# Kernel optimization log

Measured on AMD Instinct MI355X. Metric: run time of the kernel, lower is better.

Reference implementation:

```python
import jax, jax.numpy as jnp
import numpy as np

Vx, Vy, B, N, C, H, M_VIEWS = 8, 8, 4, 196, 768, 12, 4
DH = C // H
SCALE = DH ** -0.5
HID = 4 * C


def _layer_norm(x, w, b, eps=1e-5):
    mu = jnp.mean(x, axis=-1, keepdims=True)
    var = jnp.mean((x - mu) ** 2, axis=-1, keepdims=True)
    return (x - mu) / jnp.sqrt(var + eps) * w + b


def setup_inputs() -> dict:
    key = jax.random.key(0)
    ks = jax.random.split(key, 32)
    s = 0.02
    inp = {
        "xs": jax.random.normal(ks[0], (Vx, B, N, C), jnp.float32),
        "ys": jax.random.normal(ks[1], (Vy, B, N, C), jnp.float32),
        "xposes": jax.random.randint(ks[2], (Vx, B, N, 2), 0, N),
        "yposes": jax.random.randint(ks[3], (Vy, B, N, 2), 0, N),
        "rel_ids": jax.random.randint(ks[4], (Vx * M_VIEWS,), 0, Vy),
        "M": M_VIEWS,
        # self-attention params (qkv_bias=False, proj has bias)
        "qkv_w": jax.random.normal(ks[5], (3 * C, C), jnp.float32) * s,
        "attn_proj_w": jax.random.normal(ks[6], (C, C), jnp.float32) * s,
        "attn_proj_b": jnp.zeros((C,), jnp.float32),
        # cross-attention params
        "q_w": jax.random.normal(ks[7], (C, C), jnp.float32) * s,
        "k_w": jax.random.normal(ks[8], (C, C), jnp.float32) * s,
        "v_w": jax.random.normal(ks[9], (C, C), jnp.float32) * s,
        "cross_proj_w": jax.random.normal(ks[10], (C, C), jnp.float32) * s,
        "cross_proj_b": jnp.zeros((C,), jnp.float32),
        # MLP
        "fc1_w": jax.random.normal(ks[11], (HID, C), jnp.float32) * s,
        "fc1_b": jnp.zeros((HID,), jnp.float32),
        "fc2_w": jax.random.normal(ks[12], (C, HID), jnp.float32) * s,
        "fc2_b": jnp.zeros((C,), jnp.float32),
        # layer norms
        "ln1_w": jnp.ones((C,), jnp.float32), "ln1_b": jnp.zeros((C,), jnp.float32),
        "ln2_w": jnp.ones((C,), jnp.float32), "ln2_b": jnp.zeros((C,), jnp.float32),
        "ln3_w": jnp.ones((C,), jnp.float32), "ln3_b": jnp.zeros((C,), jnp.float32),
        "lny_w": jnp.ones((C,), jnp.float32), "lny_b": jnp.zeros((C,), jnp.float32),
    }
    return inp


def _forward(xs, ys, rel_ids, M,
             qkv_w, attn_proj_w, attn_proj_b,
             q_w, k_w, v_w, cross_proj_w, cross_proj_b,
             fc1_w, fc1_b, fc2_w, fc2_b,
             ln1_w, ln1_b, ln2_w, ln2_b, ln3_w, ln3_b, lny_w, lny_b):
    vx, b, nx, c = xs.shape
    vy, _, ny, _ = ys.shape
    x = xs.reshape(vx * b, nx, c)

    # ---- self-attention over each target view (rope=None) ----
    h = _layer_norm(x, ln1_w, ln1_b)
    qkv = (h @ qkv_w.T).reshape(vx * b, nx, 3, H, DH)
    q = jnp.transpose(qkv[:, :, 0], (0, 2, 1, 3))  # (VB,H,N,dh)
    k = jnp.transpose(qkv[:, :, 1], (0, 2, 1, 3))
    v = jnp.transpose(qkv[:, :, 2], (0, 2, 1, 3))
    attn = jax.nn.softmax(jnp.einsum('bhnd,bhkd->bhnk', q, k) * SCALE, axis=-1)
    o = jnp.einsum('bhnk,bhkd->bnhd', attn, v).reshape(vx * b, nx, c)
    x = x + (o @ attn_proj_w.T + attn_proj_b)

    # ---- batched multi-view cross-attention ----
    xn = _layer_norm(x.reshape(vx, b, nx, c), ln2_w, ln2_b)
    yn = _layer_norm(ys, lny_w, lny_b)
    qs = (xn @ q_w.T).reshape(vx, b, nx, H, DH)
    ks = (yn @ k_w.T).reshape(vy, b, ny, H, DH)
    vs = (yn @ v_w.T).reshape(vy, b, ny, H, DH)
    ks_r = ks[rel_ids].reshape(vx, M, b, ny, H, DH)  # index_select + group
    vs_r = vs[rel_ids].reshape(vx, M, b, ny, H, DH)
    # q is broadcast across the M group dim (no materialized expand)
    scores = jnp.einsum('vbnhd,vmbkhd->vmbhnk', qs, ks_r) * SCALE
    a = jax.nn.softmax(scores, axis=-1)
    o = jnp.einsum('vmbhnk,vmbkhd->vmbnhd', a, vs_r).reshape(vx, M, b, nx, c)
    o = o @ cross_proj_w.T + cross_proj_b  # (Vx,M,B,Nx,C)
    merged = jnp.max(o, axis=1).reshape(vx * b, nx, c)  # max-merge over M
    x = x + merged

    # ---- MLP ----
    h = _layer_norm(x, ln3_w, ln3_b)
    x = x + (jax.nn.gelu(h @ fc1_w.T + fc1_b, approximate=False) @ fc2_w.T + fc2_b)
    return x.reshape(vx, b, nx, c)


def reference(xs, ys, xposes, yposes, rel_ids, M,
              qkv_w, attn_proj_w, attn_proj_b,
              q_w, k_w, v_w, cross_proj_w, cross_proj_b,
              fc1_w, fc1_b, fc2_w, fc2_b,
              ln1_w, ln1_b, ln2_w, ln2_b, ln3_w, ln3_b, lny_w, lny_b):
    # xposes/yposes unused because rope=None in this configuration
    return _forward(xs, ys, rel_ids, M,
                    qkv_w, attn_proj_w, attn_proj_b,
                    q_w, k_w, v_w, cross_proj_w, cross_proj_b,
                    fc1_w, fc1_b, fc2_w, fc2_b,
                    ln1_w, ln1_b, ln2_w, ln2_b, ln3_w, ln3_b, lny_w, lny_b)
```

## Files before the change

### kernel.cpp

```cpp
#include <hip/hip_runtime.h>
#include <hip/hip_bf16.h>
#include <stdint.h>
#include <math.h>

#define H_ 12
#define NQ 196
#define CD 768
#define HIDD 3072
#define VX 8
#define VY 8
#define BB 4
#define MV 4
#define VBB 32
#define ROWS 6272
#define CROSS_ROWS 25088
#define SCALE_LOG2E 0.180336880260608f

typedef __attribute__((ext_vector_type(8))) short short8;
typedef __attribute__((ext_vector_type(4))) float f32x4;
typedef __attribute__((ext_vector_type(4))) unsigned short u16x4;
typedef unsigned short u16;

#define AS1 __attribute__((address_space(1)))
#define AS3 __attribute__((address_space(3)))

__device__ __forceinline__ float bf2f(u16 u){
  union { unsigned int i; float f; } v; v.i = ((unsigned int)u) << 16; return v.f;
}
__device__ __forceinline__ u16 f2bf(float f){
  union { unsigned int i; float f; } v; v.f = f;
  return (u16)((v.i + 0x7fff + ((v.i >> 16) & 1)) >> 16);
}
__device__ __forceinline__ unsigned int f2u(float f){
  union { unsigned int i; float f; } v; v.f = f; return v.i;
}

struct CastSegs {
  const float* src[7];
  u16* dst[7];
  int cum[8];
};
__global__ __launch_bounds__(256) void k_cast_all(CastSegs segs){
  int i = blockIdx.x * 256 + threadIdx.x;
  if (i >= segs.cum[7]) return;
  int s = 0;
  #pragma unroll
  for (int k = 1; k < 7; k++) s += (i >= segs.cum[k]);
  const int off = i - segs.cum[s];
  segs.dst[s][off] = f2bf(segs.src[s][off]);
}

__global__ __launch_bounds__(256) void k_ln_bf16(const float* __restrict__ x,
    const float* __restrict__ w, const float* __restrict__ b,
    u16* __restrict__ out){
  const int row = blockIdx.x;
  const int tid = threadIdx.x;
  const float* xr = x + (size_t)row * CD;
  float v0 = xr[tid], v1 = xr[tid + 256], v2 = xr[tid + 512];
  float s  = v0 + v1 + v2;
  float s2 = v0*v0 + v1*v1 + v2*v2;
  __shared__ float red[8];
  const int lane = tid & 63, wid = tid >> 6;
  #pragma unroll
  for (int o = 32; o; o >>= 1){ s += __shfl_down(s, o); s2 += __shfl_down(s2, o); }
  if (lane == 0){ red[wid] = s; red[wid + 4] = s2; }
  __syncthreads();
  if (tid == 0){
    red[0] = red[0] + red[1] + red[2] + red[3];
    red[4] = red[4] + red[5] + red[6] + red[7];
  }
  __syncthreads();
  const float mu   = red[0] * (1.f/768.f);
  const float var  = red[4] * (1.f/768.f) - mu*mu;
  const float rstd = rsqrtf(var + 1e-5f);
  u16* orow = out + (size_t)row * CD;
  orow[tid]       = f2bf((v0 - mu)*rstd*w[tid]       + b[tid]);
  orow[tid + 256] = f2bf((v1 - mu)*rstd*w[tid + 256] + b[tid + 256]);
  orow[tid + 512] = f2bf((v2 - mu)*rstd*w[tid + 512] + b[tid + 512]);
}

template<int EPI>
__global__ __launch_bounds__(256) void k_gemm_bt(
    const u16* __restrict__ A, const u16* __restrict__ B,
    float* __restrict__ Cf, u16* __restrict__ Cb,
    const float* __restrict__ bias, const float* __restrict__ resid,
    int M, int N, int K){
  __shared__ u16 As[128 * 64];
  __shared__ u16 Bs[128 * 64];
  const int tid  = threadIdx.x;
  const int lane = tid & 63;
  const int wave = tid >> 6;
  const int wr = wave >> 1, wc = wave & 1;

  const int gx = gridDim.x;
  const int nwg = gx * gridDim.y;
  const int orig = blockIdx.y * gx + blockIdx.x;
  const int q8 = nwg >> 3, r8 = nwg & 7;
  const int xcd = orig & 7, bse = orig >> 3;
  const int wg = (xcd < r8 ? xcd * (q8 + 1) : r8 * (q8 + 1) + (xcd - r8) * q8) + bse;
  const int m0 = (wg / gx) * 128, n0 = (wg % gx) * 128;

  f32x4 acc[4][4];
  #pragma unroll
  for (int i = 0; i < 4; i++)
    #pragma unroll
    for (int j = 0; j < 4; j++) acc[i][j] = (f32x4){0.f, 0.f, 0.f, 0.f};

  const int lrow = lane >> 3;
  const int lcol = ((lane & 7) ^ lrow) * 8;
  const u16* arow = A + (size_t)(m0 + wave*32 + lrow) * K + lcol;
  const u16* brow = B + (size_t)(n0 + wave*32 + lrow) * K + lcol;

  for (int k0 = 0; k0 < K; k0 += 64){
    #pragma unroll
    for (int i = 0; i < 4; i++){
      __builtin_amdgcn_global_load_lds(
        (const AS1 void*)(arow + (size_t)i*8*K + k0),
        (AS3 void*)(As + (wave*4 + i)*512), 16, 0, 0);
      __builtin_amdgcn_global_load_lds(
        (const AS1 void*)(brow + (size_t)i*8*K + k0),
        (AS3 void*)(Bs + (wave*4 + i)*512), 16, 0, 0);
    }
    __syncthreads();
    const u16* ab = As + (wr*64 + (lane & 15))*64;
    const u16* bb = Bs + (wc*64 + (lane & 15))*64;
    const int r7 = lane & 7;
    #pragma unroll
    for (int kk = 0; kk < 2; kk++){
      const int sl = (((lane >> 4) + 4*kk) ^ r7) * 8;
      short8 af[4], bfr[4];
      #pragma unroll
      for (int f = 0; f < 4; f++){
        af[f]  = *(const short8*)(ab + f*1024 + sl);
        bfr[f] = *(const short8*)(bb + f*1024 + sl);
      }
      #pragma unroll
      for (int i = 0; i < 4; i++)
        #pragma unroll
        for (int j = 0; j < 4; j++)
          acc[i][j] = __builtin_amdgcn_mfma_f32_16x16x32_bf16(af[i], bfr[j], acc[i][j], 0, 0, 0);
    }
    __syncthreads();
  }

  #pragma unroll
  for (int i = 0; i < 4; i++){
    const int rb = m0 + wr*64 + i*16 + (lane >> 4)*4;
    #pragma unroll
    for (int j = 0; j < 4; j++){
      const int col = n0 + wc*64 + j*16 + (lane & 15);
      #pragma unroll
      for (int r = 0; r < 4; r++){
        const size_t idx = (size_t)(rb + r) * N + col;
        const float v = acc[i][j][r];
        if (EPI == 0){
          Cb[idx] = f2bf(v);
        } else if (EPI == 1){
          Cf[idx] = v + bias[col] + resid[idx];
        } else if (EPI == 2){
          Cf[idx] = v + bias[col];
        } else if (EPI == 3){
          float g = v + bias[col];
          g = 0.5f * g * (1.f + erff(g * 0.70710678118654752f));
          Cb[idx] = f2bf(g);
        } else {
          Cb[idx] = f2bf(v + bias[col]);
        }
      }
    }
  }
}

template<int MODE>
__global__ __launch_bounds__(256) void k_attn_mfma(
    const u16* __restrict__ Qb, const u16* __restrict__ Kb, const u16* __restrict__ Vb,
    u16* __restrict__ Ob, const int* __restrict__ rel_ids){
  __shared__ u16 Kl[2048];
  __shared__ u16 Vt[2048];
  __shared__ u16 Pl[4][2048];

  size_t qbase, kbase, vbase, obase;
  int qstr, kstr;
  if (MODE == 0){
    const int vb = blockIdx.x / H_, h = blockIdx.x % H_;
    qbase = (size_t)vb * NQ * 2304 + h * 64; qstr = 2304;
    kbase = qbase + 768; vbase = qbase + 1536; kstr = 2304;
    obase = (size_t)vb * NQ * CD + h * 64;
  } else {
    const int h = blockIdx.x % H_; int t = blockIdx.x / H_;
    const int b = t % BB; t /= BB;
    const int m = t % MV; const int vx = t / MV;
    const int rel = rel_ids[vx * MV + m];
    qbase = ((size_t)(vx * BB + b) * NQ) * CD + h * 64; qstr = CD;
    kbase = ((size_t)(rel * BB + b) * NQ) * 1536 + h * 64; kstr = 1536;
    vbase = kbase + 768;
    obase = ((size_t)((vx * MV + m) * BB + b) * NQ) * CD + h * 64;
  }

  const int tid  = threadIdx.x;
  const int lane = tid & 63;
  const int wave = tid >> 6;
  const int lq   = lane & 15;
  const int g    = lane >> 4;

  short8 qfrag[4][2];
  #pragma unroll
  for (int qf = 0; qf < 4; qf++){
    int qrow = wave*64 + qf*16 + lq; if (qrow > 195) qrow = 195;
    const u16* qp = Qb + qbase + (size_t)qrow * qstr + g*8;
    qfrag[qf][0] = *(const short8*)(qp);
    qfrag[qf][1] = *(const short8*)(qp + 32);
  }

  f32x4 oacc[4][4];
  #pragma unroll
  for (int i = 0; i < 4; i++)
    #pragma unroll
    for (int j = 0; j < 4; j++) oacc[i][j] = (f32x4){0.f,0.f,0.f,0.f};
  float l_[4] = {0.f, 0.f, 0.f, 0.f};

  const int skey = tid >> 3;
  const int sphys = tid & 7;
  const int sslot = sphys ^ (skey & 7);
  const int vdh0 = (tid & 7) * 8;

  for (int t0 = 0; t0 < 224; t0 += 32){
    __syncthreads();
    {
      int kg = t0 + skey; if (kg > 195) kg = 195;
      __builtin_amdgcn_global_load_lds(
        (const AS1 void*)(Kb + kbase + (size_t)kg*kstr + sslot*8),
        (AS3 void*)(Kl + wave*512), 16, 0, 0);
      short8 vv = *(const short8*)(Vb + vbase + (size_t)kg*kstr + vdh0);
      #pragma unroll
      for (int j = 0; j < 8; j++){
        int dh = vdh0 + j;
        int ssw = (skey >> 3) ^ ((dh >> 3) & 3);
        Vt[dh*32 + ssw*8 + (skey & 7)] = (u16)vv[j];
      }
    }
    __syncthreads();

    f32x4 sacc[4][2];
    #pragma unroll
    for (int qf = 0; qf < 4; qf++)
      #pragma unroll
      for (int kf = 0; kf < 2; kf++) sacc[qf][kf] = (f32x4){0.f,0.f,0.f,0.f};
    #pragma unroll
    for (int kf = 0; kf < 2; kf++){
      const int key = kf*16 + lq;
      #pragma unroll
      for (int ks = 0; ks < 2; ks++){
        short8 kfrag = *(const short8*)(Kl + key*64 + (((ks<<2) + g) ^ (key & 7))*8);
        #pragma unroll
        for (int qf = 0; qf < 4; qf++)
          sacc[qf][kf] = __builtin_amdgcn_mfma_f32_16x16x32_bf16(kfrag, qfrag[qf][ks], sacc[qf][kf], 0, 0, 0);
      }
    }

    #pragma unroll
    for (int qf = 0; qf < 4; qf++){
      float p[8], ps = 0.f;
      #pragma unroll
      for (int kf = 0; kf < 2; kf++)
        #pragma unroll
        for (int r = 0; r < 4; r++){
          const int key = t0 + kf*16 + g*4 + r;
          const float e = exp2f(sacc[qf][kf][r] * SCALE_LOG2E);
          p[kf*4 + r] = (key < 196) ? e : 0.f;
          ps += p[kf*4 + r];
        }
      ps += __shfl_xor(ps, 16);
      ps += __shfl_xor(ps, 32);
      l_[qf] += ps;
      const int q = qf*16 + lq;
      #pragma unroll
      for (int kf = 0; kf < 2; kf++){
        uint2 w;
        w.x = (f2u(p[kf*4])   >> 16) | (f2u(p[kf*4+1]) & 0xffff0000u);
        w.y = (f2u(p[kf*4+2]) >> 16) | (f2u(p[kf*4+3]) & 0xffff0000u);
        const int key0 = kf*16 + g*4;
        const int ssw = (key0 >> 3) ^ (q & 3);
        *(uint2*)(Pl[wave] + q*32 + ssw*8 + (key0 & 7)) = w;
      }
    }

    short8 vfrag[4], pfrag[4];
    #pragma unroll
    for (int dhf = 0; dhf < 4; dhf++){
      const int dh = dhf*16 + lq;
      const int ssw = g ^ ((dh >> 3) & 3);
      vfrag[dhf] = *(const short8*)(Vt + dh*32 + ssw*8);
    }
    #pragma unroll
    for (int qf = 0; qf < 4; qf++){
      const int q = qf*16 + lq;
      const int ssw = g ^ (q & 3);
      pfrag[qf] = *(const short8*)(Pl[wave] + q*32 + ssw*8);
      #pragma unroll
      for (int dhf = 0; dhf < 4; dhf++)
        oacc[qf][dhf] = __builtin_amdgcn_mfma_f32_16x16x32_bf16(vfrag[dhf], pfrag[qf], oacc[qf][dhf], 0, 0, 0);
    }
  }

  #pragma unroll
  for (int qf = 0; qf < 4; qf++){
    const int qrow = wave*64 + qf*16 + lq;
    if (qrow < 196){
      const float inv = 1.f / l_[qf];
      u16* orow = Ob + obase + (size_t)qrow * CD;
      #pragma unroll
      for (int dhf = 0; dhf < 4; dhf++){
        uint2 pk;
        pk.x = (unsigned)f2bf(oacc[qf][dhf][0]*inv) | ((unsigned)f2bf(oacc[qf][dhf][1]*inv) << 16);
        pk.y = (unsigned)f2bf(oacc[qf][dhf][2]*inv) | ((unsigned)f2bf(oacc[qf][dhf][3]*inv) << 16);
        *(uint2*)(orow + dhf*16 + g*4) = pk;
      }
    }
  }
}

__global__ __launch_bounds__(256) void k_maxmerge(const u16* __restrict__ op,
                                                  float* __restrict__ x){
  const int idx = blockIdx.x * 256 + threadIdx.x;
  const int n4 = VX * BB * NQ * CD / 4;
  if (idx >= n4) return;
  const int inner = idx % (NQ * CD / 4);
  const int vb = idx / (NQ * CD / 4);
  const int vx = vb >> 2, b = vb & 3;
  const size_t ms = (size_t)BB * NQ * CD / 4;
  const size_t base = ((size_t)vx * MV * BB + b) * (NQ * CD / 4) + inner;
  const u16x4* op4 = (const u16x4*)op;
  u16x4 a0 = op4[base], a1 = op4[base + ms], a2 = op4[base + 2*ms], a3 = op4[base + 3*ms];
  float* xo = x + (size_t)idx * 4;
  #pragma unroll
  for (int j = 0; j < 4; j++){
    float v = fmaxf(fmaxf(bf2f(a0[j]), bf2f(a1[j])), fmaxf(bf2f(a2[j]), bf2f(a3[j])));
    xo[j] += v;
  }
}

extern "C" void kernel_launch(void* const* d_in, const int* in_sizes, int n_in,
                              void* d_out, int out_size, void* d_ws, size_t ws_size,
                              hipStream_t stream){
  const float* xs           = (const float*)d_in[0];
  const float* ys           = (const float*)d_in[1];
  const int*   rel_ids      = (const int*)  d_in[4];
  const float* qkv_w        = (const float*)d_in[6];
  const float* attn_proj_w  = (const float*)d_in[7];
  const float* attn_proj_b  = (const float*)d_in[8];
  const float* q_w          = (const float*)d_in[9];
  const float* k_w          = (const float*)d_in[10];
  const float* v_w          = (const float*)d_in[11];
  const float* cross_proj_w = (const float*)d_in[12];
  const float* cross_proj_b = (const float*)d_in[13];
  const float* fc1_w        = (const float*)d_in[14];
  const float* fc1_b        = (const float*)d_in[15];
  const float* fc2_w        = (const float*)d_in[16];
  const float* fc2_b        = (const float*)d_in[17];
  const float* ln1_w        = (const float*)d_in[18];
  const float* ln1_b        = (const float*)d_in[19];
  const float* ln2_w        = (const float*)d_in[20];
  const float* ln2_b        = (const float*)d_in[21];
  const float* ln3_w        = (const float*)d_in[22];
  const float* ln3_b        = (const float*)d_in[23];
  const float* lny_w        = (const float*)d_in[24];
  const float* lny_b        = (const float*)d_in[25];
  float* out = (float*)d_out;

  char* ws = (char*)d_ws;
  size_t off = 0;
  auto alloc = [&](size_t bytes) -> char* {
    char* p = ws + off; off += (bytes + 255) & ~(size_t)255; return p;
  };
  u16* wb_qkv   = (u16*)alloc((size_t)2304*768*2);
  u16* wb_aproj = (u16*)alloc((size_t)768*768*2);
  u16* wb_q     = (u16*)alloc((size_t)768*768*2);
  u16* wb_kv    = (u16*)alloc((size_t)1536*768*2);
  u16* wb_cproj = (u16*)alloc((size_t)768*768*2);
  u16* wb_fc1   = (u16*)alloc((size_t)3072*768*2);
  u16* wb_fc2   = (u16*)alloc((size_t)768*3072*2);
  float* x_ws   = (float*)alloc((size_t)ROWS*CD*4);
  u16* hbuf     = (u16*)alloc((size_t)ROWS*CD*2);
  u16* ynbuf    = (u16*)alloc((size_t)ROWS*CD*2);
  u16* o_self   = (u16*)alloc((size_t)ROWS*CD*2);
  u16* qs       = (u16*)alloc((size_t)ROWS*CD*2);
  u16* kvs      = (u16*)alloc((size_t)ROWS*1536*2);
  u16* o_cross  = (u16*)alloc((size_t)CROSS_ROWS*CD*2);
  char* un = alloc((size_t)CROSS_ROWS*CD*2);
  u16* qkvbuf = (u16*)un;
  u16* oproj  = (u16*)un;
  u16* mid    = (u16*)un;

  CastSegs segs;
  const float* srcs[7] = {qkv_w, attn_proj_w, q_w, k_w, cross_proj_w, fc1_w, fc2_w};
  u16* dsts[7] = {wb_qkv, wb_aproj, wb_q, wb_kv, wb_cproj, wb_fc1, wb_fc2};
  int lens[7]  = {2304*768, 768*768, 768*768, 768*768, 768*768, 3072*768, 3072*768};
  segs.cum[0] = 0;
  for (int i = 0; i < 7; i++){ segs.src[i] = srcs[i]; segs.dst[i] = dsts[i];
                               segs.cum[i+1] = segs.cum[i] + lens[i]; }
  k_cast_all<<<(segs.cum[7] + 255) / 256, 256, 0, stream>>>(segs);
  CastSegs segs2;
  segs2.cum[0] = 0;
  segs2.src[0] = v_w; segs2.dst[0] = wb_kv + 768*768; segs2.cum[1] = 768*768;
  for (int i = 1; i < 7; i++){ segs2.src[i] = v_w; segs2.dst[i] = wb_kv + 768*768;
                               segs2.cum[i+1] = segs2.cum[i]; }
  k_cast_all<<<(768*768 + 255) / 256, 256, 0, stream>>>(segs2);

  k_ln_bf16<<<ROWS, 256, 0, stream>>>(xs, ln1_w, ln1_b, hbuf);
  k_gemm_bt<0><<<dim3(2304/128, ROWS/128), 256, 0, stream>>>(
      hbuf, wb_qkv, nullptr, qkvbuf, nullptr, nullptr, ROWS, 2304, 768);
  k_attn_mfma<0><<<VBB * H_, 256, 0, stream>>>(qkvbuf, qkvbuf, qkvbuf, o_self, rel_ids);
  k_gemm_bt<1><<<dim3(768/128, ROWS/128), 256, 0, stream>>>(
      o_self, wb_aproj, x_ws, nullptr, attn_proj_b, xs, ROWS, 768, 768);

  k_ln_bf16<<<ROWS, 256, 0, stream>>>(x_ws, ln2_w, ln2_b, hbuf);
  k_ln_bf16<<<ROWS, 256, 0, stream>>>(ys, lny_w, lny_b, ynbuf);
  k_gemm_bt<0><<<dim3(768/128, ROWS/128), 256, 0, stream>>>(
      hbuf, wb_q, nullptr, qs, nullptr, nullptr, ROWS, 768, 768);
  k_gemm_bt<0><<<dim3(1536/128, ROWS/128), 256, 0, stream>>>(
      ynbuf, wb_kv, nullptr, kvs, nullptr, nullptr, ROWS, 1536, 768);
  k_attn_mfma<1><<<VX * MV * BB * H_, 256, 0, stream>>>(qs, kvs, kvs, o_cross, rel_ids);
  k_gemm_bt<4><<<dim3(768/128, CROSS_ROWS/128), 256, 0, stream>>>(
      o_cross, wb_cproj, nullptr, oproj, cross_proj_b, nullptr, CROSS_ROWS, 768, 768);
  k_maxmerge<<<(ROWS * CD / 4 + 255) / 256, 256, 0, stream>>>(oproj, x_ws);

  k_ln_bf16<<<ROWS, 256, 0, stream>>>(x_ws, ln3_w, ln3_b, hbuf);
  k_gemm_bt<3><<<dim3(HIDD/128, ROWS/128), 256, 0, stream>>>(
      hbuf, wb_fc1, nullptr, mid, fc1_b, nullptr, ROWS, HIDD, 768);
  k_gemm_bt<1><<<dim3(768/128, ROWS/128), 256, 0, stream>>>(
      mid, wb_fc2, out, nullptr, fc2_b, x_ws, ROWS, 768, HIDD);
}
```

Measured before the change: 422.3 us.

## Double-buffer K/V tiles and use transposed LDS reads in attention kernel

```diff
diff --git a/kernel.cpp b/kernel.cpp
--- a/kernel.cpp
+++ b/kernel.cpp
@@ -175,9 +175,8 @@
 __global__ __launch_bounds__(256) void k_attn_mfma(
     const u16* __restrict__ Qb, const u16* __restrict__ Kb, const u16* __restrict__ Vb,
     u16* __restrict__ Ob, const int* __restrict__ rel_ids){
-  __shared__ u16 Kl[2048];
-  __shared__ u16 Vt[2048];
-  __shared__ u16 Pl[4][2048];
+  __shared__ u16 Kl[2][2048];
+  __shared__ u16 Vl[2][2048];
 
   size_t qbase, kbase, vbase, obase;
   int qstr, kstr;
@@ -219,45 +218,63 @@
     for (int j = 0; j < 4; j++) oacc[i][j] = (f32x4){0.f,0.f,0.f,0.f};
   float l_[4] = {0.f, 0.f, 0.f, 0.f};
 
-  const int skey = tid >> 3;
-  const int sphys = tid & 7;
-  const int sslot = sphys ^ (skey & 7);
-  const int vdh0 = (tid & 7) * 8;
-
-  for (int t0 = 0; t0 < 224; t0 += 32){
-    __syncthreads();
-    {
-      int kg = t0 + skey; if (kg > 195) kg = 195;
-      __builtin_amdgcn_global_load_lds(
+  const int skey  = tid >> 3;
+  const int sslot = (tid & 7) ^ (skey & 7);
+  const int vkey = lane >> 1;
+  const int vdh  = wave*16 + (lane & 1)*8;
+
+  auto STAGE = [&](int nb, int t0n){
+    int kg = t0n + skey; if (kg > 195) kg = 195;
+    __builtin_amdgcn_global_load_lds(
         (const AS1 void*)(Kb + kbase + (size_t)kg*kstr + sslot*8),
-        (AS3 void*)(Kl + wave*512), 16, 0, 0);
-      short8 vv = *(const short8*)(Vb + vbase + (size_t)kg*kstr + vdh0);
-      #pragma unroll
-      for (int j = 0; j < 8; j++){
-        int dh = vdh0 + j;
-        int ssw = (skey >> 3) ^ ((dh >> 3) & 3);
-        Vt[dh*32 + ssw*8 + (skey & 7)] = (u16)vv[j];
-      }
-    }
-    __syncthreads();
+        (AS3 void*)(&Kl[nb][wave*512]), 16, 0, 0);
+    int vg = t0n + vkey; if (vg > 195) vg = 195;
+    __builtin_amdgcn_global_load_lds(
+        (const AS1 void*)(Vb + vbase + (size_t)vg*kstr + vdh),
+        (AS3 void*)(&Vl[nb][wave*512]), 16, 0, 0);
+  };
+
+  union U8 { unsigned u[4]; short8 s; };
+
+  STAGE(0, 0);
+  __syncthreads();
+
+  for (int t = 0; t < 7; t++){
+    const int cb = t & 1;
+    const int t0 = t * 32;
+    if (t < 6) STAGE(cb ^ 1, t0 + 32);
 
     f32x4 sacc[4][2];
     #pragma unroll
     for (int qf = 0; qf < 4; qf++)
       #pragma unroll
       for (int kf = 0; kf < 2; kf++) sacc[qf][kf] = (f32x4){0.f,0.f,0.f,0.f};
+    __builtin_amdgcn_s_setprio(1);
     #pragma unroll
     for (int kf = 0; kf < 2; kf++){
       const int key = kf*16 + lq;
       #pragma unroll
       for (int ks = 0; ks < 2; ks++){
-        short8 kfrag = *(const short8*)(Kl + key*64 + (((ks<<2) + g) ^ (key & 7))*8);
+        short8 kfrag = *(const short8*)(&Kl[cb][key*64 + (((ks<<2) + g) ^ (key & 7))*8]);
         #pragma unroll
         for (int qf = 0; qf < 4; qf++)
           sacc[qf][kf] = __builtin_amdgcn_mfma_f32_16x16x32_bf16(kfrag, qfrag[qf][ks], sacc[qf][kf], 0, 0, 0);
       }
     }
-
+    __builtin_amdgcn_s_setprio(0);
+
+    const AS3 u16* vp = (const AS3 u16*)(&Vl[cb][0]) + (size_t)lane*4;
+    uint2 tr0a, tr0b, tr1a, tr1b, tr2a, tr2b, tr3a, tr3b;
+    asm volatile("ds_read_b64_tr_b16 %0, %1 offset:0"    : "=&v"(tr0a) : "v"(vp));
+    asm volatile("ds_read_b64_tr_b16 %0, %1 offset:512"  : "=&v"(tr0b) : "v"(vp));
+    asm volatile("ds_read_b64_tr_b16 %0, %1 offset:1024" : "=&v"(tr1a) : "v"(vp));
+    asm volatile("ds_read_b64_tr_b16 %0, %1 offset:1536" : "=&v"(tr1b) : "v"(vp));
+    asm volatile("ds_read_b64_tr_b16 %0, %1 offset:2048" : "=&v"(tr2a) : "v"(vp));
+    asm volatile("ds_read_b64_tr_b16 %0, %1 offset:2560" : "=&v"(tr2b) : "v"(vp));
+    asm volatile("ds_read_b64_tr_b16 %0, %1 offset:3072" : "=&v"(tr3a) : "v"(vp));
+    asm volatile("ds_read_b64_tr_b16 %0, %1 offset:3584" : "=&v"(tr3b) : "v"(vp));
+
+    short8 vfrag[4];
     #pragma unroll
     for (int qf = 0; qf < 4; qf++){
       float p[8], ps = 0.f;
@@ -273,34 +290,27 @@
       ps += __shfl_xor(ps, 16);
       ps += __shfl_xor(ps, 32);
       l_[qf] += ps;
-      const int q = qf*16 + lq;
-      #pragma unroll
-      for (int kf = 0; kf < 2; kf++){
-        uint2 w;
-        w.x = (f2u(p[kf*4])   >> 16) | (f2u(p[kf*4+1]) & 0xffff0000u);
-        w.y = (f2u(p[kf*4+2]) >> 16) | (f2u(p[kf*4+3]) & 0xffff0000u);
-        const int key0 = kf*16 + g*4;
-        const int ssw = (key0 >> 3) ^ (q & 3);
-        *(uint2*)(Pl[wave] + q*32 + ssw*8 + (key0 & 7)) = w;
+      U8 pk;
+      pk.u[0] = (f2u(p[0]) >> 16) | (f2u(p[1]) & 0xffff0000u);
+      pk.u[1] = (f2u(p[2]) >> 16) | (f2u(p[3]) & 0xffff0000u);
+      pk.u[2] = (f2u(p[4]) >> 16) | (f2u(p[5]) & 0xffff0000u);
+      pk.u[3] = (f2u(p[6]) >> 16) | (f2u(p[7]) & 0xffff0000u);
+
+      if (qf == 0){
+        asm volatile("s_waitcnt lgkmcnt(0)" ::: "memory");
+        __builtin_amdgcn_sched_barrier(0);
+        U8 v0; v0.u[0]=tr0a.x; v0.u[1]=tr0a.y; v0.u[2]=tr0b.x; v0.u[3]=tr0b.y; vfrag[0]=v0.s;
+        U8 v1; v1.u[0]=tr1a.x; v1.u[1]=tr1a.y; v1.u[2]=tr1b.x; v1.u[3]=tr1b.y; vfrag[1]=v1.s;
+        U8 v2; v2.u[0]=tr2a.x; v2.u[1]=tr2a.y; v2.u[2]=tr2b.x; v2.u[3]=tr2b.y; vfrag[2]=v2.s;
+        U8 v3; v3.u[0]=tr3a.x; v3.u[1]=tr3a.y; v3.u[2]=tr3b.x; v3.u[3]=tr3b.y; vfrag[3]=v3.s;
       }
-    }
-
-    short8 vfrag[4], pfrag[4];
-    #pragma unroll
-    for (int dhf = 0; dhf < 4; dhf++){
-      const int dh = dhf*16 + lq;
-      const int ssw = g ^ ((dh >> 3) & 3);
-      vfrag[dhf] = *(const short8*)(Vt + dh*32 + ssw*8);
-    }
-    #pragma unroll
-    for (int qf = 0; qf < 4; qf++){
-      const int q = qf*16 + lq;
-      const int ssw = g ^ (q & 3);
-      pfrag[qf] = *(const short8*)(Pl[wave] + q*32 + ssw*8);
+      __builtin_amdgcn_s_setprio(1);
       #pragma unroll
       for (int dhf = 0; dhf < 4; dhf++)
-        oacc[qf][dhf] = __builtin_amdgcn_mfma_f32_16x16x32_bf16(vfrag[dhf], pfrag[qf], oacc[qf][dhf], 0, 0, 0);
-    }
+        oacc[qf][dhf] = __builtin_amdgcn_mfma_f32_16x16x32_bf16(vfrag[dhf], pk.s, oacc[qf][dhf], 0, 0, 0);
+      __builtin_amdgcn_s_setprio(0);
+    }
+    __syncthreads();
   }
 
   #pragma unroll
```

Result: faster. 413.8 us (-2.0%).
